# Kernel optimization log

Measured on AMD Instinct MI355X. Metric: run time of the kernel, lower is better.

## Reference

```python
import jax, jax.numpy as jnp
import numpy as np

NU = 100_000   # num 'user' nodes
NI = 100_000   # num 'item' nodes
E = 1_600_000  # edges per edge type
C = 128        # channels
EPS = 1e-5


def setup_inputs() -> dict:
    key = jax.random.key(0)
    ks = jax.random.split(key, 8)
    one = jnp.ones((C,), jnp.float32)
    zero = jnp.zeros((C,), jnp.float32)
    return {
        "x_user": jax.random.normal(ks[0], (NU, C), jnp.float32),
        "x_item": jax.random.normal(ks[1], (NI, C), jnp.float32),
        "ew_ui": jax.random.uniform(ks[2], (E,), jnp.float32),
        "ew_iu": jax.random.uniform(ks[3], (E,), jnp.float32),
        "ln_w_user_0": one, "ln_b_user_0": zero,
        "ln_w_user_1": one, "ln_b_user_1": zero,
        "ln_w_item_0": one, "ln_b_item_0": zero,
        "ln_w_item_1": one, "ln_b_item_1": zero,
        # edge_index[0] = source node ids, edge_index[1] = destination node ids
        "ei_ui": jnp.stack([jax.random.randint(ks[4], (E,), 0, NU),
                             jax.random.randint(ks[5], (E,), 0, NI)]),
        "ei_iu": jnp.stack([jax.random.randint(ks[6], (E,), 0, NI),
                             jax.random.randint(ks[7], (E,), 0, NU)]),
    }


def _sage_weighted(x_src, x_dst, edge_index, edge_weight, n_dst):
    # messages = x_src[src] * w ; scatter-mean over dst ; + root (x_dst)
    msgs = x_src[edge_index[0]] * edge_weight[:, None]          # [E, C]
    sums = jax.ops.segment_sum(msgs, edge_index[1], num_segments=n_dst)
    cnt = jax.ops.segment_sum(jnp.ones_like(edge_weight), edge_index[1],
                              num_segments=n_dst)
    return sums / jnp.maximum(cnt, 1.0)[:, None] + x_dst


def _layernorm(x, w, b):
    mu = jnp.mean(x, axis=-1, keepdims=True)
    var = jnp.mean(jnp.square(x - mu), axis=-1, keepdims=True)
    return (x - mu) / jnp.sqrt(var + EPS) * w + b


def reference(x_user, x_item, ew_ui, ew_iu,
              ln_w_user_0, ln_b_user_0, ln_w_user_1, ln_b_user_1,
              ln_w_item_0, ln_b_item_0, ln_w_item_1, ln_b_item_1,
              ei_ui, ei_iu):
    ln_u = [(ln_w_user_0, ln_b_user_0), (ln_w_user_1, ln_b_user_1)]
    ln_i = [(ln_w_item_0, ln_b_item_0), (ln_w_item_1, ln_b_item_1)]
    u, it = x_user, x_item
    num_layers = 2
    for layer in range(num_layers):
        # HeteroConv aggr='sum' over edge types; one edge type per dst here.
        new_u = _sage_weighted(it, u, ei_iu, ew_iu, NU)
        new_i = _sage_weighted(u, it, ei_ui, ew_ui, NI)
        u = _layernorm(new_u, *ln_u[layer])
        it = _layernorm(new_i, *ln_i[layer])
        if layer < num_layers - 1:
            u = jax.nn.relu(u)
            it = jax.nn.relu(it)
    return jnp.stack([u, it])  # [2, 100000, 128] (user, item)
```

## Files before the change

kernel.cpp:

```cpp
#include <hip/hip_runtime.h>

#define C 128
#define EPS 1e-5f

#define NPC        512
#define NPC_SHIFT  9
#define SRC_BITS   17
#define SRC_MASK   0x1FFFF
#define TILE       4096
#define BTH        512

__device__ __forceinline__ float h2f(unsigned short u) {
    union { _Float16 h; unsigned short u; } c; c.u = u; return (float)c.h;
}
__device__ __forceinline__ unsigned short f2h(float f) {
    union { _Float16 h; unsigned short u; } c; c.h = (_Float16)f; return c.u;
}

__global__ __launch_bounds__(256) void f2h_kernel(
    const float* __restrict__ in, unsigned short* __restrict__ out, int n4)
{
    int t = blockIdx.x * 256 + threadIdx.x;
    if (t < n4) {
        float4 v = ((const float4*)in)[t];
        ((ushort4*)out)[t] = make_ushort4(f2h(v.x), f2h(v.y), f2h(v.z), f2h(v.w));
    }
}

__global__ __launch_bounds__(BTH) void coarse_count_kernel(
    const int* __restrict__ ei_iu, const int* __restrict__ ei_ui,
    int* __restrict__ coarse_cnt, int E, int NU)
{
    __shared__ int hist[512];
    int tid = threadIdx.x;
    hist[tid] = 0;
    __syncthreads();
    int base = blockIdx.x * TILE;
    #pragma unroll
    for (int k = 0; k < TILE / BTH; ++k) {
        int t = base + tid + k * BTH;
        if (t < 2 * E) {
            int node;
            if (t < E) node = ei_iu[E + t];
            else       node = NU + ei_ui[E + (t - E)];
            atomicAdd(&hist[node >> NPC_SHIFT], 1);
        }
    }
    __syncthreads();
    if (hist[tid] > 0) atomicAdd(&coarse_cnt[tid], hist[tid]);
}

__global__ __launch_bounds__(512) void coarse_scan_kernel(
    const int* __restrict__ coarse_cnt, int* __restrict__ coarse_rp,
    int* __restrict__ coarse_cur, int* __restrict__ rp,
    int NCOARSE, int NTOT, int total)
{
    __shared__ int lds[512];
    int t = threadIdx.x;
    int v0 = (t < NCOARSE) ? coarse_cnt[t] : 0;
    lds[t] = v0;
    __syncthreads();
    for (int off = 1; off < 512; off <<= 1) {
        int v = (t >= off) ? lds[t - off] : 0;
        __syncthreads();
        lds[t] += v;
        __syncthreads();
    }
    int excl = lds[t] - v0;
    if (t < NCOARSE) { coarse_rp[t] = excl; coarse_cur[t] = excl; }
    if (t == 0) rp[NTOT] = total;
}

__global__ __launch_bounds__(BTH) void bin_kernel(
    const int* __restrict__ ei_iu, const float* __restrict__ ew_iu,
    const int* __restrict__ ei_ui, const float* __restrict__ ew_ui,
    int* __restrict__ coarse_cur, unsigned long long* __restrict__ binned,
    int E, int NU)
{
    __shared__ int hist[512];
    __shared__ int loff[512];
    __shared__ int cursor[512];
    __shared__ int gbase[512];
    __shared__ unsigned long long staged[TILE];
    __shared__ unsigned short sbucket[TILE];

    int tid = threadIdx.x;
    int base = blockIdx.x * TILE;
    hist[tid] = 0;
    __syncthreads();

    int cb[TILE / BTH];
    unsigned long long val[TILE / BTH];
    #pragma unroll
    for (int k = 0; k < TILE / BTH; ++k) {
        int t = base + tid + k * BTH;
        cb[k] = -1;
        if (t < 2 * E) {
            int node, src; float w;
            if (t < E) { node = ei_iu[E + t]; src = ei_iu[t]; w = ew_iu[t]; }
            else { int e = t - E; node = NU + ei_ui[E + e]; src = ei_ui[e]; w = ew_ui[e]; }
            cb[k] = node >> NPC_SHIFT;
            unsigned packed = ((unsigned)(node & (NPC - 1)) << SRC_BITS) | (unsigned)src;
            val[k] = ((unsigned long long)__float_as_uint(w) << 32) | packed;
            atomicAdd(&hist[cb[k]], 1);
        }
    }
    __syncthreads();

    loff[tid] = hist[tid];
    __syncthreads();
    for (int off = 1; off < 512; off <<= 1) {
        int v = (tid >= off) ? loff[tid - off] : 0;
        __syncthreads();
        loff[tid] += v;
        __syncthreads();
    }
    int excl = loff[tid] - hist[tid];
    __syncthreads();
    loff[tid] = excl;
    cursor[tid] = excl;
    if (hist[tid] > 0) gbase[tid] = atomicAdd(&coarse_cur[tid], hist[tid]);
    __syncthreads();

    #pragma unroll
    for (int k = 0; k < TILE / BTH; ++k) {
        if (cb[k] >= 0) {
            int j = atomicAdd(&cursor[cb[k]], 1);
            staged[j] = val[k];
            sbucket[j] = (unsigned short)cb[k];
        }
    }
    __syncthreads();

    int total = min(TILE, 2 * E - base);
    for (int j = tid; j < total; j += BTH) {
        int b = sbucket[j];
        binned[gbase[b] + (j - loff[b])] = staged[j];
    }
}

__global__ __launch_bounds__(512) void build_kernel(
    const unsigned long long* __restrict__ binned,
    const int* __restrict__ coarse_cnt, const int* __restrict__ coarse_rp,
    int* __restrict__ rp, int2* __restrict__ csr, int NTOT)
{
    __shared__ int hist[NPC];
    __shared__ int cur[NPC];
    __shared__ int ps[512];
    int cb  = blockIdx.x;
    int tid = threadIdx.x;
    int cnt  = coarse_cnt[cb];
    int base = coarse_rp[cb];
    int lo   = cb << NPC_SHIFT;
    int ncnt = min(NPC, NTOT - lo);

    hist[tid] = 0;
    __syncthreads();
    for (int j = tid; j < cnt; j += 512) {
        unsigned packed = (unsigned)(binned[base + j] & 0xFFFFFFFFu);
        atomicAdd(&hist[packed >> SRC_BITS], 1);
    }
    __syncthreads();

    int h = hist[tid];
    ps[tid] = h;
    __syncthreads();
    for (int off = 1; off < 512; off <<= 1) {
        int v = (tid >= off) ? ps[tid - off] : 0;
        __syncthreads();
        ps[tid] += v;
        __syncthreads();
    }
    int r = base + ps[tid] - h;
    if (tid < ncnt) rp[lo + tid] = r;
    cur[tid] = r;
    __syncthreads();

    for (int j = tid; j < cnt; j += 512) {
        unsigned long long v = binned[base + j];
        unsigned packed = (unsigned)(v & 0xFFFFFFFFu);
        int pos = atomicAdd(&cur[packed >> SRC_BITS], 1);
        csr[pos] = make_int2((int)(packed & SRC_MASK), (int)(v >> 32));
    }
}

__global__ __launch_bounds__(256) void sage_ln_kernel(
    const unsigned short* __restrict__ xh_src,
    const void* __restrict__ x_dst, int dst_half,
    const int* __restrict__ rp,
    const int2* __restrict__ csr,
    const float* __restrict__ lnw,
    const float* __restrict__ lnb,
    float* __restrict__ out_f,
    unsigned short* __restrict__ out_h,
    int N, int do_relu)
{
    int row  = blockIdx.x * 4 + (threadIdx.x >> 6);
    int lane = threadIdx.x & 63;
    int sub  = lane >> 5;
    int cl   = lane & 31;
    if (row >= N) return;
    int start = rp[row];
    int end   = rp[row + 1];

    float4 acc = {0.f, 0.f, 0.f, 0.f};
    for (int base = start; base < end; base += 64) {
        int idx = base + lane;
        int src = 0;
        float w = 0.0f;
        if (idx < end) {
            int2 ev = csr[idx];
            src = ev.x;
            w   = __int_as_float(ev.y);
        }
        int n  = min(64, end - base);
        int nr = (n + 7) & ~7;
        for (int j = 0; j < nr; j += 8) {
            int   s0 = __shfl(src, j + 0 + sub, 64);
            int   s1 = __shfl(src, j + 2 + sub, 64);
            int   s2 = __shfl(src, j + 4 + sub, 64);
            int   s3 = __shfl(src, j + 6 + sub, 64);
            float w0 = __shfl(w,   j + 0 + sub, 64);
            float w1 = __shfl(w,   j + 2 + sub, 64);
            float w2 = __shfl(w,   j + 4 + sub, 64);
            float w3 = __shfl(w,   j + 6 + sub, 64);
            ushort4 u0 = ((const ushort4*)(xh_src + (size_t)s0 * C))[cl];
            ushort4 u1 = ((const ushort4*)(xh_src + (size_t)s1 * C))[cl];
            ushort4 u2 = ((const ushort4*)(xh_src + (size_t)s2 * C))[cl];
            ushort4 u3 = ((const ushort4*)(xh_src + (size_t)s3 * C))[cl];
            acc.x += h2f(u0.x) * w0; acc.y += h2f(u0.y) * w0;
            acc.z += h2f(u0.z) * w0; acc.w += h2f(u0.w) * w0;
            acc.x += h2f(u1.x) * w1; acc.y += h2f(u1.y) * w1;
            acc.z += h2f(u1.z) * w1; acc.w += h2f(u1.w) * w1;
            acc.x += h2f(u2.x) * w2; acc.y += h2f(u2.y) * w2;
            acc.z += h2f(u2.z) * w2; acc.w += h2f(u2.w) * w2;
            acc.x += h2f(u3.x) * w3; acc.y += h2f(u3.y) * w3;
            acc.z += h2f(u3.z) * w3; acc.w += h2f(u3.w) * w3;
        }
    }
    acc.x += __shfl_xor(acc.x, 32, 64);
    acc.y += __shfl_xor(acc.y, 32, 64);
    acc.z += __shfl_xor(acc.z, 32, 64);
    acc.w += __shfl_xor(acc.w, 32, 64);

    float inv = 1.0f / fmaxf((float)(end - start), 1.0f);
    float4 xd;
    if (dst_half) {
        ushort4 u = ((const ushort4*)((const unsigned short*)x_dst + (size_t)row * C))[cl];
        xd = make_float4(h2f(u.x), h2f(u.y), h2f(u.z), h2f(u.w));
    } else {
        xd = ((const float4*)((const float*)x_dst + (size_t)row * C))[cl];
    }
    float4 v;
    v.x = acc.x * inv + xd.x;
    v.y = acc.y * inv + xd.y;
    v.z = acc.z * inv + xd.z;
    v.w = acc.w * inv + xd.w;

    float sum = v.x + v.y + v.z + v.w;
    float sq  = v.x * v.x + v.y * v.y + v.z * v.z + v.w * v.w;
    #pragma unroll
    for (int off = 16; off > 0; off >>= 1) {
        sum += __shfl_xor(sum, off, 64);
        sq  += __shfl_xor(sq,  off, 64);
    }
    float mu   = sum * (1.0f / C);
    float var  = sq * (1.0f / C) - mu * mu;
    float rstd = rsqrtf(var + EPS);

    float4 wv = ((const float4*)lnw)[cl];
    float4 bv = ((const float4*)lnb)[cl];
    float4 o;
    o.x = (v.x - mu) * rstd * wv.x + bv.x;
    o.y = (v.y - mu) * rstd * wv.y + bv.y;
    o.z = (v.z - mu) * rstd * wv.z + bv.z;
    o.w = (v.w - mu) * rstd * wv.w + bv.w;
    if (do_relu) {
        o.x = fmaxf(o.x, 0.f); o.y = fmaxf(o.y, 0.f);
        o.z = fmaxf(o.z, 0.f); o.w = fmaxf(o.w, 0.f);
    }
    if (sub == 0) {
        if (out_f) ((float4*)(out_f + (size_t)row * C))[cl] = o;
        if (out_h) ((ushort4*)(out_h + (size_t)row * C))[cl] =
            make_ushort4(f2h(o.x), f2h(o.y), f2h(o.z), f2h(o.w));
    }
}

extern "C" void kernel_launch(void* const* d_in, const int* in_sizes, int n_in,
                              void* d_out, int out_size, void* d_ws, size_t ws_size,
                              hipStream_t stream)
{
    const float* x_user = (const float*)d_in[0];
    const float* x_item = (const float*)d_in[1];
    const float* ew_ui  = (const float*)d_in[2];
    const float* ew_iu  = (const float*)d_in[3];
    const float* lnwu0  = (const float*)d_in[4];
    const float* lnbu0  = (const float*)d_in[5];
    const float* lnwu1  = (const float*)d_in[6];
    const float* lnbu1  = (const float*)d_in[7];
    const float* lnwi0  = (const float*)d_in[8];
    const float* lnbi0  = (const float*)d_in[9];
    const float* lnwi1  = (const float*)d_in[10];
    const float* lnbi1  = (const float*)d_in[11];
    const int*   ei_ui  = (const int*)d_in[12];
    const int*   ei_iu  = (const int*)d_in[13];

    const int NU = in_sizes[0] / C;
    const int NI = in_sizes[1] / C;
    const int E  = in_sizes[2];
    const int NTOT = NU + NI;
    const int NCOARSE = (NTOT + NPC - 1) >> NPC_SHIFT;

    float* out   = (float*)d_out;
    float* out_u = out;
    float* out_i = out + (size_t)NU * C;

    char* p = (char*)d_ws;
    unsigned short* xh_item = (unsigned short*)p;
    p += (size_t)NI * C * sizeof(unsigned short);
    size_t acth_bytes = (size_t)NU * C * sizeof(unsigned short);
    size_t binned_bytes = (size_t)2 * E * sizeof(unsigned long long);
    unsigned short* acth_u = (unsigned short*)p;
    p += (acth_bytes > binned_bytes) ? acth_bytes : binned_bytes;
    unsigned long long* binned = (unsigned long long*)acth_u;
    int2*  csr       = (int2*)p;              p += (size_t)2 * E * sizeof(int2);
    int*   rp        = (int*)p;               p += (size_t)(NTOT + 1) * sizeof(int);
    int*   coarse_cnt = (int*)p;              p += 512 * sizeof(int);
    int*   coarse_rp  = (int*)p;              p += 512 * sizeof(int);
    int*   coarse_cur = (int*)p;              p += 512 * sizeof(int);

    unsigned short* xh_user = (unsigned short*)out_u;
    unsigned short* outh_i  = xh_item;

    const int NTILE = (2 * E + TILE - 1) / TILE;

    dim3 fblk(256);
    dim3 fgrd_u((NU + 3) / 4), fgrd_i((NI + 3) / 4);

    int n4u = NU * C / 4, n4i = NI * C / 4;
    f2h_kernel<<<(n4u + 255) / 256, 256, 0, stream>>>(x_user, xh_user, n4u);
    f2h_kernel<<<(n4i + 255) / 256, 256, 0, stream>>>(x_item, xh_item, n4i);

    hipMemsetAsync(coarse_cnt, 0, 512 * sizeof(int), stream);
    coarse_count_kernel<<<NTILE, BTH, 0, stream>>>(ei_iu, ei_ui, coarse_cnt, E, NU);
    coarse_scan_kernel<<<1, 512, 0, stream>>>(coarse_cnt, coarse_rp, coarse_cur,
                                              rp, NCOARSE, NTOT, 2 * E);
    bin_kernel<<<NTILE, BTH, 0, stream>>>(ei_iu, ew_iu, ei_ui, ew_ui,
                                          coarse_cur, binned, E, NU);
    build_kernel<<<NCOARSE, 512, 0, stream>>>(binned, coarse_cnt, coarse_rp,
                                              rp, csr, NTOT);

    sage_ln_kernel<<<fgrd_u, fblk, 0, stream>>>(xh_item, x_user, 0, rp, csr,
                                                lnwu0, lnbu0, nullptr, acth_u, NU, 1);
    sage_ln_kernel<<<fgrd_i, fblk, 0, stream>>>(xh_user, x_item, 0, rp + NU, csr,
                                                lnwi0, lnbi0, nullptr, outh_i, NI, 1);

    sage_ln_kernel<<<fgrd_u, fblk, 0, stream>>>(outh_i, acth_u, 1, rp, csr,
                                                lnwu1, lnbu1, out_u, nullptr, NU, 0);
    sage_ln_kernel<<<fgrd_i, fblk, 0, stream>>>(acth_u, outh_i, 1, rp + NU, csr,
                                                lnwi1, lnbi1, out_i, nullptr, NI, 0);
}
```

Measured before the change: 584.1 us.

## Bin edges into fixed-capacity coarse buckets, dropping the separate count pass

Removes the coarse count kernel by giving each coarse bucket (now 256 nodes, 782 buckets) a fixed capacity slot in the binned buffer, so bin_kernel can scatter directly with atomic counters. The scan moves after binning and only produces row offsets for the build. It also swaps manual half-to-float unions for native half vector loads. This saves a full pass over the destination indices, but it assumes no bucket exceeds the fixed capacity and reuses the output buffer as scratch for binned edges.

Result: faster. 550.2 us (-5.8%).

```diff
diff --git a/kernel.cpp b/kernel.cpp
--- a/kernel.cpp
+++ b/kernel.cpp
@@ -3,16 +3,16 @@
 #define C 128
 #define EPS 1e-5f
 
-#define NPC        512
-#define NPC_SHIFT  9
+#define NPC        256
+#define NPC_SHIFT  8
+#define CAP        5120
 #define SRC_BITS   17
 #define SRC_MASK   0x1FFFF
 #define TILE       4096
-#define BTH        512
-
-__device__ __forceinline__ float h2f(unsigned short u) {
-    union { _Float16 h; unsigned short u; } c; c.u = u; return (float)c.h;
-}
+#define BINTH      1024
+
+typedef _Float16 half4v __attribute__((ext_vector_type(4)));
+
 __device__ __forceinline__ unsigned short f2h(float f) {
     union { _Float16 h; unsigned short u; } c; c.h = (_Float16)f; return c.u;
 }
@@ -27,60 +27,16 @@
     }
 }
 
-__global__ __launch_bounds__(BTH) void coarse_count_kernel(
-    const int* __restrict__ ei_iu, const int* __restrict__ ei_ui,
-    int* __restrict__ coarse_cnt, int E, int NU)
-{
-    __shared__ int hist[512];
-    int tid = threadIdx.x;
-    hist[tid] = 0;
-    __syncthreads();
-    int base = blockIdx.x * TILE;
-    #pragma unroll
-    for (int k = 0; k < TILE / BTH; ++k) {
-        int t = base + tid + k * BTH;
-        if (t < 2 * E) {
-            int node;
-            if (t < E) node = ei_iu[E + t];
-            else       node = NU + ei_ui[E + (t - E)];
-            atomicAdd(&hist[node >> NPC_SHIFT], 1);
-        }
-    }
-    __syncthreads();
-    if (hist[tid] > 0) atomicAdd(&coarse_cnt[tid], hist[tid]);
-}
-
-__global__ __launch_bounds__(512) void coarse_scan_kernel(
-    const int* __restrict__ coarse_cnt, int* __restrict__ coarse_rp,
-    int* __restrict__ coarse_cur, int* __restrict__ rp,
-    int NCOARSE, int NTOT, int total)
-{
-    __shared__ int lds[512];
-    int t = threadIdx.x;
-    int v0 = (t < NCOARSE) ? coarse_cnt[t] : 0;
-    lds[t] = v0;
-    __syncthreads();
-    for (int off = 1; off < 512; off <<= 1) {
-        int v = (t >= off) ? lds[t - off] : 0;
-        __syncthreads();
-        lds[t] += v;
-        __syncthreads();
-    }
-    int excl = lds[t] - v0;
-    if (t < NCOARSE) { coarse_rp[t] = excl; coarse_cur[t] = excl; }
-    if (t == 0) rp[NTOT] = total;
-}
-
-__global__ __launch_bounds__(BTH) void bin_kernel(
+__global__ __launch_bounds__(BINTH) void bin_kernel(
     const int* __restrict__ ei_iu, const float* __restrict__ ew_iu,
     const int* __restrict__ ei_ui, const float* __restrict__ ew_ui,
-    int* __restrict__ coarse_cur, unsigned long long* __restrict__ binned,
+    int* __restrict__ coarse_cnt, unsigned long long* __restrict__ binned,
     int E, int NU)
 {
-    __shared__ int hist[512];
-    __shared__ int loff[512];
-    __shared__ int cursor[512];
-    __shared__ int gbase[512];
+    __shared__ int hist[BINTH];
+    __shared__ int loff[BINTH];
+    __shared__ int cursor[BINTH];
+    __shared__ int gbase[BINTH];
     __shared__ unsigned long long staged[TILE];
     __shared__ unsigned short sbucket[TILE];
 
@@ -89,11 +45,11 @@
     hist[tid] = 0;
     __syncthreads();
 
-    int cb[TILE / BTH];
-    unsigned long long val[TILE / BTH];
+    int cb[TILE / BINTH];
+    unsigned long long val[TILE / BINTH];
     #pragma unroll
-    for (int k = 0; k < TILE / BTH; ++k) {
-        int t = base + tid + k * BTH;
+    for (int k = 0; k < TILE / BINTH; ++k) {
+        int t = base + tid + k * BINTH;
         cb[k] = -1;
         if (t < 2 * E) {
             int node, src; float w;
@@ -109,7 +65,7 @@
 
     loff[tid] = hist[tid];
     __syncthreads();
-    for (int off = 1; off < 512; off <<= 1) {
+    for (int off = 1; off < BINTH; off <<= 1) {
         int v = (tid >= off) ? loff[tid - off] : 0;
         __syncthreads();
         loff[tid] += v;
@@ -119,11 +75,12 @@
     __syncthreads();
     loff[tid] = excl;
     cursor[tid] = excl;
-    if (hist[tid] > 0) gbase[tid] = atomicAdd(&coarse_cur[tid], hist[tid]);
+    if (hist[tid] > 0)
+        gbase[tid] = tid * CAP + atomicAdd(&coarse_cnt[tid], hist[tid]);
     __syncthreads();
 
     #pragma unroll
-    for (int k = 0; k < TILE / BTH; ++k) {
+    for (int k = 0; k < TILE / BINTH; ++k) {
         if (cb[k] >= 0) {
             int j = atomicAdd(&cursor[cb[k]], 1);
             staged[j] = val[k];
@@ -133,10 +90,29 @@
     __syncthreads();
 
     int total = min(TILE, 2 * E - base);
-    for (int j = tid; j < total; j += BTH) {
+    for (int j = tid; j < total; j += BINTH) {
         int b = sbucket[j];
         binned[gbase[b] + (j - loff[b])] = staged[j];
     }
+}
+
+__global__ __launch_bounds__(1024) void coarse_scan_kernel(
+    const int* __restrict__ coarse_cnt, int* __restrict__ coarse_rp,
+    int* __restrict__ rp, int NCOARSE, int NTOT, int total)
+{
+    __shared__ int lds[1024];
+    int t = threadIdx.x;
+    int v0 = (t < NCOARSE) ? coarse_cnt[t] : 0;
+    lds[t] = v0;
+    __syncthreads();
+    for (int off = 1; off < 1024; off <<= 1) {
+        int v = (t >= off) ? lds[t - off] : 0;
+        __syncthreads();
+        lds[t] += v;
+        __syncthreads();
+    }
+    if (t < NCOARSE) coarse_rp[t] = lds[t] - v0;
+    if (t == 0) rp[NTOT] = total;
 }
 
 __global__ __launch_bounds__(512) void build_kernel(
@@ -146,38 +122,41 @@
 {
     __shared__ int hist[NPC];
     __shared__ int cur[NPC];
-    __shared__ int ps[512];
+    __shared__ int ps[NPC];
     int cb  = blockIdx.x;
     int tid = threadIdx.x;
-    int cnt  = coarse_cnt[cb];
-    int base = coarse_rp[cb];
-    int lo   = cb << NPC_SHIFT;
-    int ncnt = min(NPC, NTOT - lo);
-
-    hist[tid] = 0;
+    int cnt   = coarse_cnt[cb];
+    int rbase = coarse_rp[cb];
+    int gb    = cb * CAP;
+    int lo    = cb << NPC_SHIFT;
+    int ncnt  = min(NPC, NTOT - lo);
+
+    if (tid < NPC) hist[tid] = 0;
     __syncthreads();
     for (int j = tid; j < cnt; j += 512) {
-        unsigned packed = (unsigned)(binned[base + j] & 0xFFFFFFFFu);
+        unsigned packed = (unsigned)(binned[gb + j] & 0xFFFFFFFFu);
         atomicAdd(&hist[packed >> SRC_BITS], 1);
     }
     __syncthreads();
 
-    int h = hist[tid];
-    ps[tid] = h;
-    __syncthreads();
-    for (int off = 1; off < 512; off <<= 1) {
-        int v = (tid >= off) ? ps[tid - off] : 0;
-        __syncthreads();
-        ps[tid] += v;
-        __syncthreads();
-    }
-    int r = base + ps[tid] - h;
-    if (tid < ncnt) rp[lo + tid] = r;
-    cur[tid] = r;
+    int h = 0;
+    if (tid < NPC) { h = hist[tid]; ps[tid] = h; }
+    __syncthreads();
+    for (int off = 1; off < NPC; off <<= 1) {
+        int v = (tid >= off && tid < NPC) ? ps[tid - off] : 0;
+        __syncthreads();
+        if (tid < NPC) ps[tid] += v;
+        __syncthreads();
+    }
+    if (tid < NPC) {
+        int r = rbase + ps[tid] - h;
+        if (tid < ncnt) rp[lo + tid] = r;
+        cur[tid] = r;
+    }
     __syncthreads();
 
     for (int j = tid; j < cnt; j += 512) {
-        unsigned long long v = binned[base + j];
+        unsigned long long v = binned[gb + j];
         unsigned packed = (unsigned)(v & 0xFFFFFFFFu);
         int pos = atomicAdd(&cur[packed >> SRC_BITS], 1);
         csr[pos] = make_int2((int)(packed & SRC_MASK), (int)(v >> 32));
@@ -224,18 +203,18 @@
             float w1 = __shfl(w,   j + 2 + sub, 64);
             float w2 = __shfl(w,   j + 4 + sub, 64);
             float w3 = __shfl(w,   j + 6 + sub, 64);
-            ushort4 u0 = ((const ushort4*)(xh_src + (size_t)s0 * C))[cl];
-            ushort4 u1 = ((const ushort4*)(xh_src + (size_t)s1 * C))[cl];
-            ushort4 u2 = ((const ushort4*)(xh_src + (size_t)s2 * C))[cl];
-            ushort4 u3 = ((const ushort4*)(xh_src + (size_t)s3 * C))[cl];
-            acc.x += h2f(u0.x) * w0; acc.y += h2f(u0.y) * w0;
-            acc.z += h2f(u0.z) * w0; acc.w += h2f(u0.w) * w0;
-            acc.x += h2f(u1.x) * w1; acc.y += h2f(u1.y) * w1;
-            acc.z += h2f(u1.z) * w1; acc.w += h2f(u1.w) * w1;
-            acc.x += h2f(u2.x) * w2; acc.y += h2f(u2.y) * w2;
-            acc.z += h2f(u2.z) * w2; acc.w += h2f(u2.w) * w2;
-            acc.x += h2f(u3.x) * w3; acc.y += h2f(u3.y) * w3;
-            acc.z += h2f(u3.z) * w3; acc.w += h2f(u3.w) * w3;
+            half4v u0 = ((const half4v*)(xh_src + (size_t)s0 * C))[cl];
+            half4v u1 = ((const half4v*)(xh_src + (size_t)s1 * C))[cl];
+            half4v u2 = ((const half4v*)(xh_src + (size_t)s2 * C))[cl];
+            half4v u3 = ((const half4v*)(xh_src + (size_t)s3 * C))[cl];
+            acc.x += (float)u0[0] * w0; acc.y += (float)u0[1] * w0;
+            acc.z += (float)u0[2] * w0; acc.w += (float)u0[3] * w0;
+            acc.x += (float)u1[0] * w1; acc.y += (float)u1[1] * w1;
+            acc.z += (float)u1[2] * w1; acc.w += (float)u1[3] * w1;
+            acc.x += (float)u2[0] * w2; acc.y += (float)u2[1] * w2;
+            acc.z += (float)u2[2] * w2; acc.w += (float)u2[3] * w2;
+            acc.x += (float)u3[0] * w3; acc.y += (float)u3[1] * w3;
+            acc.z += (float)u3[2] * w3; acc.w += (float)u3[3] * w3;
         }
     }
     acc.x += __shfl_xor(acc.x, 32, 64);
@@ -246,8 +225,8 @@
     float inv = 1.0f / fmaxf((float)(end - start), 1.0f);
     float4 xd;
     if (dst_half) {
-        ushort4 u = ((const ushort4*)((const unsigned short*)x_dst + (size_t)row * C))[cl];
-        xd = make_float4(h2f(u.x), h2f(u.y), h2f(u.z), h2f(u.w));
+        half4v u = ((const half4v*)((const unsigned short*)x_dst + (size_t)row * C))[cl];
+        xd = make_float4((float)u[0], (float)u[1], (float)u[2], (float)u[3]);
     } else {
         xd = ((const float4*)((const float*)x_dst + (size_t)row * C))[cl];
     }
@@ -318,18 +297,15 @@
     char* p = (char*)d_ws;
     unsigned short* xh_item = (unsigned short*)p;
     p += (size_t)NI * C * sizeof(unsigned short);
-    size_t acth_bytes = (size_t)NU * C * sizeof(unsigned short);
-    size_t binned_bytes = (size_t)2 * E * sizeof(unsigned long long);
     unsigned short* acth_u = (unsigned short*)p;
-    p += (acth_bytes > binned_bytes) ? acth_bytes : binned_bytes;
-    unsigned long long* binned = (unsigned long long*)acth_u;
-    int2*  csr       = (int2*)p;              p += (size_t)2 * E * sizeof(int2);
-    int*   rp        = (int*)p;               p += (size_t)(NTOT + 1) * sizeof(int);
-    int*   coarse_cnt = (int*)p;              p += 512 * sizeof(int);
-    int*   coarse_rp  = (int*)p;              p += 512 * sizeof(int);
-    int*   coarse_cur = (int*)p;              p += 512 * sizeof(int);
+    p += (size_t)NU * C * sizeof(unsigned short);
+    int2*  csr        = (int2*)p;             p += (size_t)2 * E * sizeof(int2);
+    int*   rp         = (int*)p;              p += (size_t)(NTOT + 1) * sizeof(int);
+    int*   coarse_cnt = (int*)p;              p += 1024 * sizeof(int);
+    int*   coarse_rp  = (int*)p;              p += 1024 * sizeof(int);
 
     unsigned short* xh_user = (unsigned short*)out_u;
+    unsigned long long* binned = (unsigned long long*)out_i;
     unsigned short* outh_i  = xh_item;
 
     const int NTILE = (2 * E + TILE - 1) / TILE;
@@ -341,12 +317,11 @@
     f2h_kernel<<<(n4u + 255) / 256, 256, 0, stream>>>(x_user, xh_user, n4u);
     f2h_kernel<<<(n4i + 255) / 256, 256, 0, stream>>>(x_item, xh_item, n4i);
 
-    hipMemsetAsync(coarse_cnt, 0, 512 * sizeof(int), stream);
-    coarse_count_kernel<<<NTILE, BTH, 0, stream>>>(ei_iu, ei_ui, coarse_cnt, E, NU);
-    coarse_scan_kernel<<<1, 512, 0, stream>>>(coarse_cnt, coarse_rp, coarse_cur,
-                                              rp, NCOARSE, NTOT, 2 * E);
-    bin_kernel<<<NTILE, BTH, 0, stream>>>(ei_iu, ew_iu, ei_ui, ew_ui,
-                                          coarse_cur, binned, E, NU);
+    hipMemsetAsync(coarse_cnt, 0, 1024 * sizeof(int), stream);
+    bin_kernel<<<NTILE, BINTH, 0, stream>>>(ei_iu, ew_iu, ei_ui, ew_ui,
+                                            coarse_cnt, binned, E, NU);
+    coarse_scan_kernel<<<1, 1024, 0, stream>>>(coarse_cnt, coarse_rp,
+                                               rp, NCOARSE, NTOT, 2 * E);
     build_kernel<<<NCOARSE, 512, 0, stream>>>(binned, coarse_cnt, coarse_rp,
                                               rp, csr, NTOT);
 
```
